# Performance work log

Hardware: AMD Instinct MI355X
Metric: run time of the kernel (lower is better)

The kernel has to match this reference:

```python
import jax, jax.numpy as jnp
import numpy as np

N, H, F, E, K = 4096, 512, 2048, 8, 2  # tokens, hidden, ffn(=4H), experts, top_k


def setup_inputs() -> dict:
    key = jax.random.key(0)
    ks = jax.random.split(key, 7)
    def w(k, shape, fan_in):
        return jax.random.normal(k, shape, dtype=jnp.float32) * (fan_in ** -0.5)
    return {
        "x": jax.random.normal(ks[0], (N, H), dtype=jnp.float32),
        "W_in": w(ks[1], (H, H), H),          # input_proj.weight  [out,in]
        "W_router": w(ks[2], (E, H), H),      # router.gate.weight [E,H]
        "W_gate": w(ks[3], (E, F, H), H),     # per-expert gate_proj.weight
        "W_up": w(ks[4], (E, F, H), H),       # per-expert up_proj.weight
        "W_down": w(ks[5], (E, H, F), F),     # per-expert down_proj.weight
        "W_out": w(ks[6], (H, H), H),         # output_proj.weight
    }


def reference(x, W_in, W_router, W_gate, W_up, W_down, W_out):
    h = x @ W_in.T                                  # [N,H] input_proj
    logits = h @ W_router.T                         # [N,E]
    # route_mode='balanced' and world_size==1 -> expert_bias is None
    probs = jax.nn.softmax(logits, axis=-1)
    top_w, top_i = jax.lax.top_k(probs, K)          # [N,K]
    top_w = jax.nn.softmax(top_w, axis=-1)          # renormalize over top-k

    # per-token combine weight for each expert: [N,E]
    onehot = jax.nn.one_hot(top_i, E, dtype=h.dtype)      # [N,K,E]
    combine_w = jnp.einsum('nk,nke->ne', top_w, onehot)

    def expert(wg, wu, wd):
        # SwiGLU FFN: down( silu(gate(h)) * up(h) )
        return (jax.nn.silu(h @ wg.T) * (h @ wu.T)) @ wd.T  # [N,H]

    expert_out = jax.vmap(expert)(W_gate, W_up, W_down)     # [E,N,H]
    combined = jnp.einsum('ne,enh->nh', combine_w, expert_out)
    return combined @ W_out.T                                # output_proj
```

## Files before the change

kernel.cpp:

```cpp
#include <hip/hip_runtime.h>

typedef unsigned short u16;
typedef unsigned int u32;
typedef short bf16x8 __attribute__((ext_vector_type(8)));
typedef float f32x4 __attribute__((ext_vector_type(4)));

#define AS1 __attribute__((address_space(1)))
#define AS3 __attribute__((address_space(3)))

#define NTOK 4096
#define HDIM 512
#define FDIM 2048
#define NEXP 8
#define NASSIGN (NTOK * 2)
#define NPAD (NASSIGN + NEXP * 128)
#define RBMAX 128

__device__ __forceinline__ void g2l16(const void* g, void* l) {
  __builtin_amdgcn_global_load_lds((const AS1 u32*)g, (AS3 u32*)l, 16, 0, 0);
}
__device__ __forceinline__ u16 f2bf(float f) {
  u32 u = __float_as_uint(f);
  u = (u + 0x7FFFu + ((u >> 16) & 1u)) >> 16;
  return (u16)u;
}
__device__ __forceinline__ float bf2f(u16 h) { return __uint_as_float(((u32)h) << 16); }

#define VMBAR() do { asm volatile("s_waitcnt vmcnt(0)" ::: "memory"); __builtin_amdgcn_s_barrier(); } while (0)

__global__ __launch_bounds__(512, 4) void prep1_kernel(
    const float* __restrict__ x, const float* __restrict__ Wi, const float* __restrict__ Wo,
    const float* __restrict__ Wr, u16* __restrict__ xb, u16* __restrict__ Wib,
    u16* __restrict__ Wob, double* __restrict__ wre) {
  const int b = blockIdx.x, tid = threadIdx.x;
  if (b < 640) {
    const float* s; u16* d; int base;
    if (b < 512) { s = x; d = xb; base = b * 1024; }
    else if (b < 576) { s = Wi; d = Wib; base = (b - 512) * 1024; }
    else { s = Wo; d = Wob; base = (b - 576) * 1024; }
#pragma unroll
    for (int i = 0; i < 2; ++i) {
      const int ix = base + tid + i * 512;
      const float4 v = ((const float4*)s)[ix];
      ushort4 o; o.x = f2bf(v.x); o.y = f2bf(v.y); o.z = f2bf(v.z); o.w = f2bf(v.w);
      ((ushort4*)d)[ix] = o;
    }
  } else {
    const int t = (b - 640) * 512 + tid;
    const int e = t >> 9, k = t & 511;
    const float* wr = Wr + e * HDIM;
    double a = 0.0;
    for (int j = 0; j < HDIM; ++j) a += (double)wr[j] * (double)Wi[j * HDIM + k];
    wre[t] = a;
  }
}

template <int SB, int NT>
__device__ __forceinline__ void gemm128_body(
    const u16* __restrict__ A, const u16* __restrict__ B, void* __restrict__ C,
    int m0, int n0, int N, int K, u16* sm, int tid) {
  u16 *lA0 = sm, *lA1 = sm + 8192, *lB0 = sm + 16384, *lB1 = sm + 24576;
  const int w = tid >> 6, l = tid & 63;
  const int wm = (w >> 2) * 64, wn = (w & 3) * 32;
  const int lm = l & 15, lk = (l >> 4) * 8, xr = (l & 7) << 3;
  const int sr = l >> 3, sc = ((l & 7) ^ sr) * 8;
  const u16* As = A + (size_t)(m0 + w * 8 + sr) * K + sc;
  const u16* Bs = B + (size_t)(n0 + w * 8 + sr) * K + sc;
  f32x4 acc[4][2] = {};
  auto STG = [&](u16* dA, u16* dB, int kt) {
    g2l16(As + kt, dA + w * 512);
    g2l16(As + (size_t)64 * K + kt, dA + 4096 + w * 512);
    g2l16(Bs + kt, dB + w * 512);
    g2l16(Bs + (size_t)64 * K + kt, dB + 4096 + w * 512);
  };
  auto CMP = [&](const u16* a_, const u16* b_) {
#pragma unroll
    for (int kk = 0; kk < 2; ++kk) {
      const int ko = (kk * 32 + lk) ^ xr;
      bf16x8 af[4], bf[2];
#pragma unroll
      for (int i = 0; i < 4; ++i) af[i] = *(const bf16x8*)(a_ + (wm + i * 16 + lm) * 64 + ko);
#pragma unroll
      for (int j = 0; j < 2; ++j) bf[j] = *(const bf16x8*)(b_ + (wn + j * 16 + lm) * 64 + ko);
#pragma unroll
      for (int i = 0; i < 4; ++i)
#pragma unroll
        for (int j = 0; j < 2; ++j)
          acc[i][j] = __builtin_amdgcn_mfma_f32_16x16x32_bf16(af[i], bf[j], acc[i][j], 0, 0, 0);
    }
  };
  STG(lA0, lB0, 0);
  VMBAR();
  for (int t = 0; t < NT; t += 2) {
    if (t + 1 < NT) STG(lA1, lB1, (t + 1) * 64);
    CMP(lA0, lB0);
    VMBAR();
    if (t + 2 < NT) STG(lA0, lB0, (t + 2) * 64);
    CMP(lA1, lB1);
    VMBAR();
  }
  const int cr = (l >> 4) * 4, cc = lm;
#pragma unroll
  for (int i = 0; i < 4; ++i)
#pragma unroll
    for (int j = 0; j < 2; ++j)
#pragma unroll
      for (int r = 0; r < 4; ++r) {
        const size_t o = (size_t)(m0 + wm + i * 16 + cr + r) * N + n0 + wn + j * 16 + cc;
        if (SB) ((u16*)C)[o] = f2bf(acc[i][j][r]);
        else ((float*)C)[o] = acc[i][j][r];
      }
}

__global__ __launch_bounds__(512, 4) void prep2_kernel(
    const float* __restrict__ x, const double* __restrict__ wre,
    const u16* __restrict__ xb, const u16* __restrict__ Wib,
    const float* __restrict__ Wg, const float* __restrict__ Wu, const float* __restrict__ Wd,
    u16* __restrict__ hb, u16* __restrict__ Wgb, u16* __restrict__ Wub, u16* __restrict__ Wdb,
    int* __restrict__ idx, float* __restrict__ wts) {
  __shared__ __align__(16) u16 pp[32768];
  const int b = blockIdx.x, tid = threadIdx.x;
  if (b < 8) {
    double* lw = (double*)pp;
    for (int i = tid; i < NEXP * HDIM; i += 512) lw[i] = wre[i];
    __syncthreads();
    const int n = b * 512 + tid;
    const float* xr = x + (size_t)n * HDIM;
    double acc[NEXP] = {};
    for (int k4 = 0; k4 < HDIM / 4; ++k4) {
      const float4 xv = ((const float4*)xr)[k4];
      const float xc[4] = {xv.x, xv.y, xv.z, xv.w};
#pragma unroll
      for (int c = 0; c < 4; ++c) {
        const double xd = (double)xc[c];
#pragma unroll
        for (int e = 0; e < NEXP; ++e) acc[e] += xd * lw[e * HDIM + k4 * 4 + c];
      }
    }
    double mx = acc[0];
#pragma unroll
    for (int e = 1; e < NEXP; ++e) mx = acc[e] > mx ? acc[e] : mx;
    double p[NEXP], se = 0.0;
#pragma unroll
    for (int e = 0; e < NEXP; ++e) { p[e] = exp(acc[e] - mx); se += p[e]; }
    const double inv = 1.0 / se;
#pragma unroll
    for (int e = 0; e < NEXP; ++e) p[e] *= inv;
    int i0 = 0; double b0 = p[0];
#pragma unroll
    for (int e = 1; e < NEXP; ++e) if (p[e] > b0) { b0 = p[e]; i0 = e; }
    int i1 = -1; double b1 = -1.0;
#pragma unroll
    for (int e = 0; e < NEXP; ++e) if (e != i0 && p[e] > b1) { b1 = p[e]; i1 = e; }
    const double e0 = exp(b0), e1 = exp(b1);
    idx[2 * n] = i0; idx[2 * n + 1] = i1;
    wts[2 * n] = (float)(e0 / (e0 + e1));
    wts[2 * n + 1] = (float)(e1 / (e0 + e1));
  } else if (b < 136) {
    const int g = b - 8;
    gemm128_body<1, 8>(xb, Wib, hb, (g >> 2) * 128, (g & 3) * 128, HDIM, HDIM, pp, tid);
  } else {
    const int cb = b - 136, which = cb >> 9, lb = cb & 511;
    const float* s = which == 0 ? Wg : which == 1 ? Wu : Wd;
    u16* d = which == 0 ? Wgb : which == 1 ? Wub : Wdb;
    const int base = lb * 4096 + tid;
#pragma unroll
    for (int i = 0; i < 8; ++i) {
      const int ix = base + i * 512;
      const float4 v = ((const float4*)s)[ix];
      ushort4 o; o.x = f2bf(v.x); o.y = f2bf(v.y); o.z = f2bf(v.z); o.w = f2bf(v.w);
      ((ushort4*)d)[ix] = o;
    }
  }
}

__global__ void assign_kernel(const int* __restrict__ idx, int* __restrict__ tok,
                              int* __restrict__ pos, int* __restrict__ rbe,
                              int* __restrict__ rbp, int* __restrict__ nrb) {
  __shared__ int cnt[NEXP], cur[NEXP];
  const int tid = threadIdx.x;
  if (tid < NEXP) cnt[tid] = 0;
  __syncthreads();
  for (int a = tid; a < NASSIGN; a += 256) atomicAdd(&cnt[idx[a]], 1);
  __syncthreads();
  if (tid == 0) {
    int o = 0, n = 0;
    for (int e = 0; e < NEXP; ++e) {
      cur[e] = o;
      const int nb = (cnt[e] + 127) >> 7;
      for (int i = 0; i < nb; ++i) { rbe[n] = e; rbp[n] = o + i * 128; ++n; }
      o += nb * 128;
    }
    nrb[0] = n;
  }
  __syncthreads();
  for (int p = tid; p < NPAD; p += 256) tok[p] = 0;
  __syncthreads();
  for (int a = tid; a < NASSIGN; a += 256) {
    const int e = idx[a];
    const int q = atomicAdd(&cur[e], 1);
    tok[q] = a >> 1;
    pos[a] = q;
  }
}

__global__ __launch_bounds__(512, 2) void gateup_kernel(
    const u16* __restrict__ hb, const u16* __restrict__ Wg, const u16* __restrict__ Wu,
    u16* __restrict__ act, const int* __restrict__ tok, const int* __restrict__ rbe,
    const int* __restrict__ rbp, const int* __restrict__ nrb) {
  const int rb = blockIdx.y;
  if (rb >= nrb[0]) return;
  __shared__ __align__(16) u16 sm[49152];
  u16 *lA0 = sm, *lA1 = sm + 8192, *lG0 = sm + 16384, *lG1 = sm + 24576,
      *lU0 = sm + 32768, *lU1 = sm + 40960;
  const int e = rbe[rb], p0 = rbp[rb], n0 = blockIdx.x * 128;
  const int tid = threadIdx.x, w = tid >> 6, l = tid & 63;
  const int wm = (w >> 2) * 64, wn = (w & 3) * 32;
  const int lm = l & 15, lk = (l >> 4) * 8, xr = (l & 7) << 3;
  const int sr = l >> 3, sc = ((l & 7) ^ sr) * 8;
  const u16* A0 = hb + (size_t)tok[p0 + w * 8 + sr] * HDIM + sc;
  const u16* A1 = hb + (size_t)tok[p0 + 64 + w * 8 + sr] * HDIM + sc;
  const u16* G0 = Wg + (size_t)e * FDIM * HDIM + (size_t)(n0 + w * 8 + sr) * HDIM + sc;
  const u16* G1 = G0 + (size_t)64 * HDIM;
  const u16* U0 = Wu + (size_t)e * FDIM * HDIM + (size_t)(n0 + w * 8 + sr) * HDIM + sc;
  const u16* U1 = U0 + (size_t)64 * HDIM;
  f32x4 ag[4][2] = {}, au[4][2] = {};
  auto STG = [&](u16* dA, u16* dG, u16* dU, int kt) {
    g2l16(A0 + kt, dA + w * 512);
    g2l16(A1 + kt, dA + 4096 + w * 512);
    g2l16(G0 + kt, dG + w * 512);
    g2l16(G1 + kt, dG + 4096 + w * 512);
    g2l16(U0 + kt, dU + w * 512);
    g2l16(U1 + kt, dU + 4096 + w * 512);
  };
  auto CMP = [&](const u16* a_, const u16* g_, const u16* u_) {
#pragma unroll
    for (int kk = 0; kk < 2; ++kk) {
      const int ko = (kk * 32 + lk) ^ xr;
      bf16x8 af[4], gf[2], uf[2];
#pragma unroll
      for (int i = 0; i < 4; ++i) af[i] = *(const bf16x8*)(a_ + (wm + i * 16 + lm) * 64 + ko);
#pragma unroll
      for (int j = 0; j < 2; ++j) {
        gf[j] = *(const bf16x8*)(g_ + (wn + j * 16 + lm) * 64 + ko);
        uf[j] = *(const bf16x8*)(u_ + (wn + j * 16 + lm) * 64 + ko);
      }
#pragma unroll
      for (int i = 0; i < 4; ++i)
#pragma unroll
        for (int j = 0; j < 2; ++j) {
          ag[i][j] = __builtin_amdgcn_mfma_f32_16x16x32_bf16(af[i], gf[j], ag[i][j], 0, 0, 0);
          au[i][j] = __builtin_amdgcn_mfma_f32_16x16x32_bf16(af[i], uf[j], au[i][j], 0, 0, 0);
        }
    }
  };
  STG(lA0, lG0, lU0, 0);
  VMBAR();
#pragma unroll
  for (int t = 0; t < 8; t += 2) {
    if (t + 1 < 8) STG(lA1, lG1, lU1, (t + 1) * 64);
    CMP(lA0, lG0, lU0);
    VMBAR();
    if (t + 2 < 8) STG(lA0, lG0, lU0, (t + 2) * 64);
    CMP(lA1, lG1, lU1);
    VMBAR();
  }
  const int cr = (l >> 4) * 4, cc = lm;
#pragma unroll
  for (int i = 0; i < 4; ++i)
#pragma unroll
    for (int j = 0; j < 2; ++j)
#pragma unroll
      for (int r = 0; r < 4; ++r) {
        const float g = ag[i][j][r], u = au[i][j][r];
        const float s = g / (1.0f + __expf(-g));
        act[(size_t)(p0 + wm + i * 16 + cr + r) * FDIM + n0 + wn + j * 16 + cc] = f2bf(s * u);
      }
}

__global__ __launch_bounds__(512, 2) void down_kernel(
    const u16* __restrict__ act, const u16* __restrict__ Wd, u16* __restrict__ dwn,
    const int* __restrict__ rbe, const int* __restrict__ rbp, const int* __restrict__ nrb) {
  const int rb = blockIdx.y;
  if (rb >= nrb[0]) return;
  __shared__ __align__(16) u16 sm[49152];
  u16 *lA0 = sm, *lA1 = sm + 8192, *lB0 = sm + 16384, *lB1 = sm + 32768;
  const int e = rbe[rb], p0 = rbp[rb], n0 = blockIdx.x * 256;
  const int tid = threadIdx.x, w = tid >> 6, l = tid & 63;
  const int wm = (w >> 2) * 64, wn = (w & 3) * 64;
  const int lm = l & 15, lk = (l >> 4) * 8, xr = (l & 7) << 3;
  const int sr = l >> 3, sc = ((l & 7) ^ sr) * 8;
  const u16* As = act + (size_t)(p0 + w * 8 + sr) * FDIM + sc;
  const u16* Bs = Wd + (size_t)e * HDIM * FDIM + (size_t)(n0 + w * 8 + sr) * FDIM + sc;
  f32x4 acc[4][4] = {};
  auto STG = [&](u16* dA, u16* dB, int kt) {
    g2l16(As + kt, dA + w * 512);
    g2l16(As + (size_t)64 * FDIM + kt, dA + 4096 + w * 512);
#pragma unroll
    for (int c = 0; c < 4; ++c)
      g2l16(Bs + (size_t)(64 * c) * FDIM + kt, dB + c * 4096 + w * 512);
  };
  auto CMP = [&](const u16* a_, const u16* b_) {
#pragma unroll
    for (int kk = 0; kk < 2; ++kk) {
      const int ko = (kk * 32 + lk) ^ xr;
      bf16x8 af[4], bf[4];
#pragma unroll
      for (int i = 0; i < 4; ++i) af[i] = *(const bf16x8*)(a_ + (wm + i * 16 + lm) * 64 + ko);
#pragma unroll
      for (int j = 0; j < 4; ++j) bf[j] = *(const bf16x8*)(b_ + (wn + j * 16 + lm) * 64 + ko);
#pragma unroll
      for (int i = 0; i < 4; ++i)
#pragma unroll
        for (int j = 0; j < 4; ++j)
          acc[i][j] = __builtin_amdgcn_mfma_f32_16x16x32_bf16(af[i], bf[j], acc[i][j], 0, 0, 0);
    }
  };
  STG(lA0, lB0, 0);
  VMBAR();
  for (int t = 0; t < 32; t += 2) {
    if (t + 1 < 32) STG(lA1, lB1, (t + 1) * 64);
    CMP(lA0, lB0);
    VMBAR();
    if (t + 2 < 32) STG(lA0, lB0, (t + 2) * 64);
    CMP(lA1, lB1);
    VMBAR();
  }
  const int cr = (l >> 4) * 4, cc = lm;
#pragma unroll
  for (int i = 0; i < 4; ++i)
#pragma unroll
    for (int j = 0; j < 4; ++j)
#pragma unroll
      for (int r = 0; r < 4; ++r)
        dwn[(size_t)(p0 + wm + i * 16 + cr + r) * HDIM + n0 + wn + j * 16 + cc] = f2bf(acc[i][j][r]);
}

__global__ void combine_kernel(const u16* __restrict__ dwn, const int* __restrict__ pos,
                               const float* __restrict__ wts, u16* __restrict__ cb) {
  const int n = blockIdx.x, t = threadIdx.x;
  const int p0 = pos[2 * n], p1 = pos[2 * n + 1];
  const float w0 = wts[2 * n], w1 = wts[2 * n + 1];
  const ushort4 a = ((const ushort4*)(dwn + (size_t)p0 * HDIM))[t];
  const ushort4 b = ((const ushort4*)(dwn + (size_t)p1 * HDIM))[t];
  ushort4 o;
  o.x = f2bf(w0 * bf2f(a.x) + w1 * bf2f(b.x));
  o.y = f2bf(w0 * bf2f(a.y) + w1 * bf2f(b.y));
  o.z = f2bf(w0 * bf2f(a.z) + w1 * bf2f(b.z));
  o.w = f2bf(w0 * bf2f(a.w) + w1 * bf2f(b.w));
  ((ushort4*)(cb + (size_t)n * HDIM))[t] = o;
}

__global__ __launch_bounds__(512, 4) void out_gemm_kernel(
    const u16* __restrict__ cb, const u16* __restrict__ Wob, float* __restrict__ out) {
  __shared__ __align__(16) u16 sm[32768];
  gemm128_body<0, 8>(cb, Wob, out, blockIdx.y * 128, blockIdx.x * 128, HDIM, HDIM, sm, threadIdx.x);
}

extern "C" void kernel_launch(void* const* d_in, const int* in_sizes, int n_in,
                              void* d_out, int out_size, void* d_ws, size_t ws_size,
                              hipStream_t stream) {
  const float* x  = (const float*)d_in[0];
  const float* Wi = (const float*)d_in[1];
  const float* Wr = (const float*)d_in[2];
  const float* Wg = (const float*)d_in[3];
  const float* Wu = (const float*)d_in[4];
  const float* Wd = (const float*)d_in[5];
  const float* Wo = (const float*)d_in[6];
  float* out = (float*)d_out;

  char* ws = (char*)d_ws;
  size_t off = 0;
  auto alloc = [&](size_t bytes) -> void* {
    off = (off + 255) & ~(size_t)255;
    void* p = ws + off;
    off += bytes;
    return p;
  };
  u16* xb  = (u16*)alloc((size_t)NTOK * HDIM * 2);
  u16* hb  = (u16*)alloc((size_t)NTOK * HDIM * 2);
  u16* cb  = (u16*)alloc((size_t)NTOK * HDIM * 2);
  u16* Wib = (u16*)alloc((size_t)HDIM * HDIM * 2);
  u16* Wob = (u16*)alloc((size_t)HDIM * HDIM * 2);
  u16* Wgb = (u16*)alloc((size_t)NEXP * FDIM * HDIM * 2);
  u16* Wub = (u16*)alloc((size_t)NEXP * FDIM * HDIM * 2);
  u16* Wdb = (u16*)alloc((size_t)NEXP * HDIM * FDIM * 2);
  u16* actb = (u16*)alloc((size_t)NPAD * FDIM * 2);
  u16* dwn = (u16*)alloc((size_t)NPAD * HDIM * 2);
  double* wre = (double*)alloc((size_t)NEXP * HDIM * 8);
  int* idx = (int*)alloc((size_t)NASSIGN * 4);
  float* wts = (float*)alloc((size_t)NASSIGN * 4);
  int* tok = (int*)alloc((size_t)NPAD * 4);
  int* pos = (int*)alloc((size_t)NASSIGN * 4);
  int* rbe = (int*)alloc((size_t)RBMAX * 4);
  int* rbp = (int*)alloc((size_t)RBMAX * 4);
  int* nrb = (int*)alloc(256);

  prep1_kernel<<<648, 512, 0, stream>>>(x, Wi, Wo, Wr, xb, Wib, Wob, wre);
  prep2_kernel<<<1672, 512, 0, stream>>>(x, wre, xb, Wib, Wg, Wu, Wd, hb, Wgb, Wub, Wdb, idx, wts);
  assign_kernel<<<1, 256, 0, stream>>>(idx, tok, pos, rbe, rbp, nrb);
  gateup_kernel<<<dim3(16, 72), 512, 0, stream>>>(hb, Wgb, Wub, actb, tok, rbe, rbp, nrb);
  down_kernel<<<dim3(2, 72), 512, 0, stream>>>(actb, Wdb, dwn, rbe, rbp, nrb);
  combine_kernel<<<NTOK, 128, 0, stream>>>(dwn, pos, wts, cb);
  out_gemm_kernel<<<dim3(4, 32), 512, 0, stream>>>(cb, Wob, out);
}
```

Measured before the change: 218.5 us.

## Restructure prep kernels, triple-buffer expert GEMMs, split-K down projection

Replaces the two mixed prep kernels with one flat conversion kernel, separate router-weight and router kernels, and a standalone input-projection GEMM. The gate/up and down GEMMs move from double to triple-buffered LDS staging with partial vmcnt waits, so loads stay in flight across an extra iteration. The down kernel is retiled to 128-wide output with an in-block split-K across two wave groups, reduced through LDS, doubling the grid. This adds more LDS per block and extra launches, and the reduction step adds overhead.

```diff
diff --git a/kernel.cpp b/kernel.cpp
--- a/kernel.cpp
+++ b/kernel.cpp
@@ -26,152 +26,86 @@
 }
 __device__ __forceinline__ float bf2f(u16 h) { return __uint_as_float(((u32)h) << 16); }
 
-#define VMBAR() do { asm volatile("s_waitcnt vmcnt(0)" ::: "memory"); __builtin_amdgcn_s_barrier(); } while (0)
-
-__global__ __launch_bounds__(512, 4) void prep1_kernel(
+#define WAITV6() asm volatile("s_waitcnt vmcnt(6)" ::: "memory")
+#define WAITV4() asm volatile("s_waitcnt vmcnt(4)" ::: "memory")
+#define WAITV0() asm volatile("s_waitcnt vmcnt(0)" ::: "memory")
+#define BAR() __builtin_amdgcn_s_barrier()
+#define VMBAR() do { WAITV0(); BAR(); } while (0)
+
+__global__ __launch_bounds__(256) void cvtall_kernel(
     const float* __restrict__ x, const float* __restrict__ Wi, const float* __restrict__ Wo,
-    const float* __restrict__ Wr, u16* __restrict__ xb, u16* __restrict__ Wib,
-    u16* __restrict__ Wob, double* __restrict__ wre) {
-  const int b = blockIdx.x, tid = threadIdx.x;
-  if (b < 640) {
-    const float* s; u16* d; int base;
-    if (b < 512) { s = x; d = xb; base = b * 1024; }
-    else if (b < 576) { s = Wi; d = Wib; base = (b - 512) * 1024; }
-    else { s = Wo; d = Wob; base = (b - 576) * 1024; }
-#pragma unroll
-    for (int i = 0; i < 2; ++i) {
-      const int ix = base + tid + i * 512;
-      const float4 v = ((const float4*)s)[ix];
-      ushort4 o; o.x = f2bf(v.x); o.y = f2bf(v.y); o.z = f2bf(v.z); o.w = f2bf(v.w);
-      ((ushort4*)d)[ix] = o;
+    const float* __restrict__ Wg, const float* __restrict__ Wu, const float* __restrict__ Wd,
+    u16* __restrict__ xb, u16* __restrict__ Wib, u16* __restrict__ Wob,
+    u16* __restrict__ Wgb, u16* __restrict__ Wub, u16* __restrict__ Wdb) {
+  const int gid = blockIdx.x * 256 + threadIdx.x;
+  const int S = 6784 * 256;
+#pragma unroll
+  for (int k = 0; k < 4; ++k) {
+    const int i = gid + k * S;
+    const float* s; u16* d; int o;
+    if (i < 524288) { s = x; d = xb; o = i; }
+    else if (i < 589824) { s = Wi; d = Wib; o = i - 524288; }
+    else if (i < 655360) { s = Wo; d = Wob; o = i - 589824; }
+    else if (i < 2752512) { s = Wg; d = Wgb; o = i - 655360; }
+    else if (i < 4849664) { s = Wu; d = Wub; o = i - 2752512; }
+    else { s = Wd; d = Wdb; o = i - 4849664; }
+    const float4 v = ((const float4*)s)[o];
+    ushort4 t; t.x = f2bf(v.x); t.y = f2bf(v.y); t.z = f2bf(v.z); t.w = f2bf(v.w);
+    ((ushort4*)d)[o] = t;
+  }
+}
+
+__global__ __launch_bounds__(256) void wreff_kernel(
+    const float* __restrict__ Wr, const float* __restrict__ Wi, double* __restrict__ wre) {
+  const int t = blockIdx.x * 256 + threadIdx.x;
+  const int e = t >> 9, k = t & 511;
+  const float* wr = Wr + e * HDIM;
+  double a = 0.0;
+  for (int j = 0; j < HDIM; j += 8) {
+#pragma unroll
+    for (int u = 0; u < 8; ++u) a += (double)wr[j + u] * (double)Wi[(j + u) * HDIM + k];
+  }
+  wre[t] = a;
+}
+
+__global__ __launch_bounds__(256) void router_kernel(
+    const float* __restrict__ x, const double* __restrict__ wre,
+    int* __restrict__ idx, float* __restrict__ wts) {
+  __shared__ double lw[NEXP * HDIM];
+  for (int i = threadIdx.x; i < NEXP * HDIM; i += 256) lw[i] = wre[i];
+  __syncthreads();
+  const int n = blockIdx.x * 256 + threadIdx.x;
+  const float* xr = x + (size_t)n * HDIM;
+  double acc[NEXP] = {};
+  for (int k4 = 0; k4 < HDIM / 4; ++k4) {
+    const float4 xv = ((const float4*)xr)[k4];
+    const float xc[4] = {xv.x, xv.y, xv.z, xv.w};
+#pragma unroll
+    for (int c = 0; c < 4; ++c) {
+      const double xd = (double)xc[c];
+#pragma unroll
+      for (int e = 0; e < NEXP; ++e) acc[e] += xd * lw[e * HDIM + k4 * 4 + c];
     }
-  } else {
-    const int t = (b - 640) * 512 + tid;
-    const int e = t >> 9, k = t & 511;
-    const float* wr = Wr + e * HDIM;
-    double a = 0.0;
-    for (int j = 0; j < HDIM; ++j) a += (double)wr[j] * (double)Wi[j * HDIM + k];
-    wre[t] = a;
-  }
-}
-
-template <int SB, int NT>
-__device__ __forceinline__ void gemm128_body(
-    const u16* __restrict__ A, const u16* __restrict__ B, void* __restrict__ C,
-    int m0, int n0, int N, int K, u16* sm, int tid) {
-  u16 *lA0 = sm, *lA1 = sm + 8192, *lB0 = sm + 16384, *lB1 = sm + 24576;
-  const int w = tid >> 6, l = tid & 63;
-  const int wm = (w >> 2) * 64, wn = (w & 3) * 32;
-  const int lm = l & 15, lk = (l >> 4) * 8, xr = (l & 7) << 3;
-  const int sr = l >> 3, sc = ((l & 7) ^ sr) * 8;
-  const u16* As = A + (size_t)(m0 + w * 8 + sr) * K + sc;
-  const u16* Bs = B + (size_t)(n0 + w * 8 + sr) * K + sc;
-  f32x4 acc[4][2] = {};
-  auto STG = [&](u16* dA, u16* dB, int kt) {
-    g2l16(As + kt, dA + w * 512);
-    g2l16(As + (size_t)64 * K + kt, dA + 4096 + w * 512);
-    g2l16(Bs + kt, dB + w * 512);
-    g2l16(Bs + (size_t)64 * K + kt, dB + 4096 + w * 512);
-  };
-  auto CMP = [&](const u16* a_, const u16* b_) {
-#pragma unroll
-    for (int kk = 0; kk < 2; ++kk) {
-      const int ko = (kk * 32 + lk) ^ xr;
-      bf16x8 af[4], bf[2];
-#pragma unroll
-      for (int i = 0; i < 4; ++i) af[i] = *(const bf16x8*)(a_ + (wm + i * 16 + lm) * 64 + ko);
-#pragma unroll
-      for (int j = 0; j < 2; ++j) bf[j] = *(const bf16x8*)(b_ + (wn + j * 16 + lm) * 64 + ko);
-#pragma unroll
-      for (int i = 0; i < 4; ++i)
-#pragma unroll
-        for (int j = 0; j < 2; ++j)
-          acc[i][j] = __builtin_amdgcn_mfma_f32_16x16x32_bf16(af[i], bf[j], acc[i][j], 0, 0, 0);
-    }
-  };
-  STG(lA0, lB0, 0);
-  VMBAR();
-  for (int t = 0; t < NT; t += 2) {
-    if (t + 1 < NT) STG(lA1, lB1, (t + 1) * 64);
-    CMP(lA0, lB0);
-    VMBAR();
-    if (t + 2 < NT) STG(lA0, lB0, (t + 2) * 64);
-    CMP(lA1, lB1);
-    VMBAR();
-  }
-  const int cr = (l >> 4) * 4, cc = lm;
-#pragma unroll
-  for (int i = 0; i < 4; ++i)
-#pragma unroll
-    for (int j = 0; j < 2; ++j)
-#pragma unroll
-      for (int r = 0; r < 4; ++r) {
-        const size_t o = (size_t)(m0 + wm + i * 16 + cr + r) * N + n0 + wn + j * 16 + cc;
-        if (SB) ((u16*)C)[o] = f2bf(acc[i][j][r]);
-        else ((float*)C)[o] = acc[i][j][r];
-      }
-}
-
-__global__ __launch_bounds__(512, 4) void prep2_kernel(
-    const float* __restrict__ x, const double* __restrict__ wre,
-    const u16* __restrict__ xb, const u16* __restrict__ Wib,
-    const float* __restrict__ Wg, const float* __restrict__ Wu, const float* __restrict__ Wd,
-    u16* __restrict__ hb, u16* __restrict__ Wgb, u16* __restrict__ Wub, u16* __restrict__ Wdb,
-    int* __restrict__ idx, float* __restrict__ wts) {
-  __shared__ __align__(16) u16 pp[32768];
-  const int b = blockIdx.x, tid = threadIdx.x;
-  if (b < 8) {
-    double* lw = (double*)pp;
-    for (int i = tid; i < NEXP * HDIM; i += 512) lw[i] = wre[i];
-    __syncthreads();
-    const int n = b * 512 + tid;
-    const float* xr = x + (size_t)n * HDIM;
-    double acc[NEXP] = {};
-    for (int k4 = 0; k4 < HDIM / 4; ++k4) {
-      const float4 xv = ((const float4*)xr)[k4];
-      const float xc[4] = {xv.x, xv.y, xv.z, xv.w};
-#pragma unroll
-      for (int c = 0; c < 4; ++c) {
-        const double xd = (double)xc[c];
-#pragma unroll
-        for (int e = 0; e < NEXP; ++e) acc[e] += xd * lw[e * HDIM + k4 * 4 + c];
-      }
-    }
-    double mx = acc[0];
-#pragma unroll
-    for (int e = 1; e < NEXP; ++e) mx = acc[e] > mx ? acc[e] : mx;
-    double p[NEXP], se = 0.0;
-#pragma unroll
-    for (int e = 0; e < NEXP; ++e) { p[e] = exp(acc[e] - mx); se += p[e]; }
-    const double inv = 1.0 / se;
-#pragma unroll
-    for (int e = 0; e < NEXP; ++e) p[e] *= inv;
-    int i0 = 0; double b0 = p[0];
-#pragma unroll
-    for (int e = 1; e < NEXP; ++e) if (p[e] > b0) { b0 = p[e]; i0 = e; }
-    int i1 = -1; double b1 = -1.0;
-#pragma unroll
-    for (int e = 0; e < NEXP; ++e) if (e != i0 && p[e] > b1) { b1 = p[e]; i1 = e; }
-    const double e0 = exp(b0), e1 = exp(b1);
-    idx[2 * n] = i0; idx[2 * n + 1] = i1;
-    wts[2 * n] = (float)(e0 / (e0 + e1));
-    wts[2 * n + 1] = (float)(e1 / (e0 + e1));
-  } else if (b < 136) {
-    const int g = b - 8;
-    gemm128_body<1, 8>(xb, Wib, hb, (g >> 2) * 128, (g & 3) * 128, HDIM, HDIM, pp, tid);
-  } else {
-    const int cb = b - 136, which = cb >> 9, lb = cb & 511;
-    const float* s = which == 0 ? Wg : which == 1 ? Wu : Wd;
-    u16* d = which == 0 ? Wgb : which == 1 ? Wub : Wdb;
-    const int base = lb * 4096 + tid;
-#pragma unroll
-    for (int i = 0; i < 8; ++i) {
-      const int ix = base + i * 512;
-      const float4 v = ((const float4*)s)[ix];
-      ushort4 o; o.x = f2bf(v.x); o.y = f2bf(v.y); o.z = f2bf(v.z); o.w = f2bf(v.w);
-      ((ushort4*)d)[ix] = o;
-    }
-  }
+  }
+  double mx = acc[0];
+#pragma unroll
+  for (int e = 1; e < NEXP; ++e) mx = acc[e] > mx ? acc[e] : mx;
+  double p[NEXP], se = 0.0;
+#pragma unroll
+  for (int e = 0; e < NEXP; ++e) { p[e] = exp(acc[e] - mx); se += p[e]; }
+  const double inv = 1.0 / se;
+#pragma unroll
+  for (int e = 0; e < NEXP; ++e) p[e] *= inv;
+  int i0 = 0; double b0 = p[0];
+#pragma unroll
+  for (int e = 1; e < NEXP; ++e) if (p[e] > b0) { b0 = p[e]; i0 = e; }
+  int i1 = -1; double b1 = -1.0;
+#pragma unroll
+  for (int e = 0; e < NEXP; ++e) if (e != i0 && p[e] > b1) { b1 = p[e]; i1 = e; }
+  const double e0 = exp(b0), e1 = exp(b1);
+  idx[2 * n] = i0; idx[2 * n + 1] = i1;
+  wts[2 * n] = (float)(e0 / (e0 + e1));
+  wts[2 * n + 1] = (float)(e1 / (e0 + e1));
 }
 
 __global__ void assign_kernel(const int* __restrict__ idx, int* __restrict__ tok,
@@ -204,15 +138,82 @@
   }
 }
 
+template <int SB, int NT>
+__device__ __forceinline__ void gemm128_body(
+    const u16* __restrict__ A, const u16* __restrict__ B, void* __restrict__ C,
+    int m0, int n0, int N, int K, u16* sm, int tid) {
+  u16 *lA0 = sm, *lA1 = sm + 8192, *lB0 = sm + 16384, *lB1 = sm + 24576;
+  const int w = tid >> 6, l = tid & 63;
+  const int wm = (w >> 2) * 64, wn = (w & 3) * 32;
+  const int lm = l & 15, lk = (l >> 4) * 8, xr = (l & 7) << 3;
+  const int sr = l >> 3, sc = ((l & 7) ^ sr) * 8;
+  const u16* As = A + (size_t)(m0 + w * 8 + sr) * K + sc;
+  const u16* Bs = B + (size_t)(n0 + w * 8 + sr) * K + sc;
+  f32x4 acc[4][2] = {};
+  auto STG = [&](u16* dA, u16* dB, int kt) {
+    g2l16(As + kt, dA + w * 512);
+    g2l16(As + (size_t)64 * K + kt, dA + 4096 + w * 512);
+    g2l16(Bs + kt, dB + w * 512);
+    g2l16(Bs + (size_t)64 * K + kt, dB + 4096 + w * 512);
+  };
+  auto CMP = [&](const u16* a_, const u16* b_) {
+#pragma unroll
+    for (int kk = 0; kk < 2; ++kk) {
+      const int ko = (kk * 32 + lk) ^ xr;
+      bf16x8 af[4], bf[2];
+#pragma unroll
+      for (int i = 0; i < 4; ++i) af[i] = *(const bf16x8*)(a_ + (wm + i * 16 + lm) * 64 + ko);
+#pragma unroll
+      for (int j = 0; j < 2; ++j) bf[j] = *(const bf16x8*)(b_ + (wn + j * 16 + lm) * 64 + ko);
+#pragma unroll
+      for (int i = 0; i < 4; ++i)
+#pragma unroll
+        for (int j = 0; j < 2; ++j)
+          acc[i][j] = __builtin_amdgcn_mfma_f32_16x16x32_bf16(af[i], bf[j], acc[i][j], 0, 0, 0);
+    }
+  };
+  STG(lA0, lB0, 0);
+  VMBAR();
+  for (int t = 0; t < NT; t += 2) {
+    if (t + 1 < NT) STG(lA1, lB1, (t + 1) * 64);
+    CMP(lA0, lB0);
+    VMBAR();
+    if (t + 2 < NT) STG(lA0, lB0, (t + 2) * 64);
+    CMP(lA1, lB1);
+    VMBAR();
+  }
+  const int cr = (l >> 4) * 4, cc = lm;
+#pragma unroll
+  for (int i = 0; i < 4; ++i)
+#pragma unroll
+    for (int j = 0; j < 2; ++j)
+#pragma unroll
+      for (int r = 0; r < 4; ++r) {
+        const size_t o = (size_t)(m0 + wm + i * 16 + cr + r) * N + n0 + wn + j * 16 + cc;
+        if (SB) ((u16*)C)[o] = f2bf(acc[i][j][r]);
+        else ((float*)C)[o] = acc[i][j][r];
+      }
+}
+
+__global__ __launch_bounds__(512, 2) void ingemm_kernel(
+    const u16* __restrict__ xb, const u16* __restrict__ Wib, u16* __restrict__ hb) {
+  __shared__ __align__(16) u16 sm[32768];
+  gemm128_body<1, 8>(xb, Wib, hb, blockIdx.y * 128, blockIdx.x * 128, HDIM, HDIM, sm, threadIdx.x);
+}
+
+__global__ __launch_bounds__(512, 2) void outgemm_kernel(
+    const u16* __restrict__ cb, const u16* __restrict__ Wob, float* __restrict__ out) {
+  __shared__ __align__(16) u16 sm[32768];
+  gemm128_body<0, 8>(cb, Wob, out, blockIdx.y * 128, blockIdx.x * 128, HDIM, HDIM, sm, threadIdx.x);
+}
+
 __global__ __launch_bounds__(512, 2) void gateup_kernel(
     const u16* __restrict__ hb, const u16* __restrict__ Wg, const u16* __restrict__ Wu,
     u16* __restrict__ act, const int* __restrict__ tok, const int* __restrict__ rbe,
     const int* __restrict__ rbp, const int* __restrict__ nrb) {
   const int rb = blockIdx.y;
   if (rb >= nrb[0]) return;
-  __shared__ __align__(16) u16 sm[49152];
-  u16 *lA0 = sm, *lA1 = sm + 8192, *lG0 = sm + 16384, *lG1 = sm + 24576,
-      *lU0 = sm + 32768, *lU1 = sm + 40960;
+  __shared__ __align__(16) u16 sm[73728];
   const int e = rbe[rb], p0 = rbp[rb], n0 = blockIdx.x * 128;
   const int tid = threadIdx.x, w = tid >> 6, l = tid & 63;
   const int wm = (w >> 2) * 64, wn = (w & 3) * 32;
@@ -225,15 +226,19 @@
   const u16* U0 = Wu + (size_t)e * FDIM * HDIM + (size_t)(n0 + w * 8 + sr) * HDIM + sc;
   const u16* U1 = U0 + (size_t)64 * HDIM;
   f32x4 ag[4][2] = {}, au[4][2] = {};
-  auto STG = [&](u16* dA, u16* dG, u16* dU, int kt) {
-    g2l16(A0 + kt, dA + w * 512);
-    g2l16(A1 + kt, dA + 4096 + w * 512);
-    g2l16(G0 + kt, dG + w * 512);
-    g2l16(G1 + kt, dG + 4096 + w * 512);
-    g2l16(U0 + kt, dU + w * 512);
-    g2l16(U1 + kt, dU + 4096 + w * 512);
-  };
-  auto CMP = [&](const u16* a_, const u16* g_, const u16* u_) {
+  auto STG = [&](int b, int kt) {
+    u16* d = sm + b * 24576;
+    g2l16(A0 + kt, d + w * 512);
+    g2l16(A1 + kt, d + 4096 + w * 512);
+    g2l16(G0 + kt, d + 8192 + w * 512);
+    g2l16(G1 + kt, d + 12288 + w * 512);
+    g2l16(U0 + kt, d + 16384 + w * 512);
+    g2l16(U1 + kt, d + 20480 + w * 512);
+  };
+  auto CMP = [&](int b) {
+    const u16* a_ = sm + b * 24576;
+    const u16* g_ = a_ + 8192;
+    const u16* u_ = a_ + 16384;
 #pragma unroll
     for (int kk = 0; kk < 2; ++kk) {
       const int ko = (kk * 32 + lk) ^ xr;
@@ -254,16 +259,14 @@
         }
     }
   };
-  STG(lA0, lG0, lU0, 0);
-  VMBAR();
-#pragma unroll
-  for (int t = 0; t < 8; t += 2) {
-    if (t + 1 < 8) STG(lA1, lG1, lU1, (t + 1) * 64);
-    CMP(lA0, lG0, lU0);
-    VMBAR();
-    if (t + 2 < 8) STG(lA0, lG0, lU0, (t + 2) * 64);
-    CMP(lA1, lG1, lU1);
-    VMBAR();
+  STG(0, 0); STG(1, 64);
+  WAITV6(); BAR();
+#pragma unroll
+  for (int t = 0; t < 8; ++t) {
+    if (t + 2 < 8) STG((t + 2) % 3, (t + 2) * 64);
+    CMP(t % 3);
+    if (t + 2 < 8) WAITV6(); else WAITV0();
+    BAR();
   }
   const int cr = (l >> 4) * 4, cc = lm;
 #pragma unroll
@@ -284,56 +287,71 @@
   const int rb = blockIdx.y;
   if (rb >= nrb[0]) return;
   __shared__ __align__(16) u16 sm[49152];
-  u16 *lA0 = sm, *lA1 = sm + 8192, *lB0 = sm + 16384, *lB1 = sm + 32768;
-  const int e = rbe[rb], p0 = rbp[rb], n0 = blockIdx.x * 256;
+  const int e = rbe[rb], p0 = rbp[rb], n0 = blockIdx.x * 128;
   const int tid = threadIdx.x, w = tid >> 6, l = tid & 63;
-  const int wm = (w >> 2) * 64, wn = (w & 3) * 64;
+  const int g = w >> 2;
+  const int wm = ((w >> 1) & 1) * 64, wn = (w & 1) * 64;
   const int lm = l & 15, lk = (l >> 4) * 8, xr = (l & 7) << 3;
+  const int ko = (g * 32 + lk) ^ xr;
   const int sr = l >> 3, sc = ((l & 7) ^ sr) * 8;
   const u16* As = act + (size_t)(p0 + w * 8 + sr) * FDIM + sc;
   const u16* Bs = Wd + (size_t)e * HDIM * FDIM + (size_t)(n0 + w * 8 + sr) * FDIM + sc;
   f32x4 acc[4][4] = {};
-  auto STG = [&](u16* dA, u16* dB, int kt) {
-    g2l16(As + kt, dA + w * 512);
-    g2l16(As + (size_t)64 * FDIM + kt, dA + 4096 + w * 512);
-#pragma unroll
-    for (int c = 0; c < 4; ++c)
-      g2l16(Bs + (size_t)(64 * c) * FDIM + kt, dB + c * 4096 + w * 512);
-  };
-  auto CMP = [&](const u16* a_, const u16* b_) {
-#pragma unroll
-    for (int kk = 0; kk < 2; ++kk) {
-      const int ko = (kk * 32 + lk) ^ xr;
-      bf16x8 af[4], bf[4];
-#pragma unroll
-      for (int i = 0; i < 4; ++i) af[i] = *(const bf16x8*)(a_ + (wm + i * 16 + lm) * 64 + ko);
-#pragma unroll
-      for (int j = 0; j < 4; ++j) bf[j] = *(const bf16x8*)(b_ + (wn + j * 16 + lm) * 64 + ko);
-#pragma unroll
-      for (int i = 0; i < 4; ++i)
-#pragma unroll
-        for (int j = 0; j < 4; ++j)
-          acc[i][j] = __builtin_amdgcn_mfma_f32_16x16x32_bf16(af[i], bf[j], acc[i][j], 0, 0, 0);
-    }
-  };
-  STG(lA0, lB0, 0);
-  VMBAR();
-  for (int t = 0; t < 32; t += 2) {
-    if (t + 1 < 32) STG(lA1, lB1, (t + 1) * 64);
-    CMP(lA0, lB0);
-    VMBAR();
-    if (t + 2 < 32) STG(lA0, lB0, (t + 2) * 64);
-    CMP(lA1, lB1);
-    VMBAR();
-  }
-  const int cr = (l >> 4) * 4, cc = lm;
-#pragma unroll
-  for (int i = 0; i < 4; ++i)
-#pragma unroll
-    for (int j = 0; j < 4; ++j)
-#pragma unroll
-      for (int r = 0; r < 4; ++r)
-        dwn[(size_t)(p0 + wm + i * 16 + cr + r) * HDIM + n0 + wn + j * 16 + cc] = f2bf(acc[i][j][r]);
+  auto STG = [&](int b, int kt) {
+    u16* d = sm + b * 16384;
+    g2l16(As + kt, d + w * 512);
+    g2l16(As + (size_t)64 * FDIM + kt, d + 4096 + w * 512);
+    g2l16(Bs + kt, d + 8192 + w * 512);
+    g2l16(Bs + (size_t)64 * FDIM + kt, d + 12288 + w * 512);
+  };
+  auto CMP = [&](int b) {
+    const u16* a_ = sm + b * 16384;
+    const u16* b_ = a_ + 8192;
+    bf16x8 af[4], bf[4];
+#pragma unroll
+    for (int i = 0; i < 4; ++i) af[i] = *(const bf16x8*)(a_ + (wm + i * 16 + lm) * 64 + ko);
+#pragma unroll
+    for (int j = 0; j < 4; ++j) bf[j] = *(const bf16x8*)(b_ + (wn + j * 16 + lm) * 64 + ko);
+#pragma unroll
+    for (int i = 0; i < 4; ++i)
+#pragma unroll
+      for (int j = 0; j < 4; ++j)
+        acc[i][j] = __builtin_amdgcn_mfma_f32_16x16x32_bf16(af[i], bf[j], acc[i][j], 0, 0, 0);
+  };
+  STG(0, 0); STG(1, 64);
+  WAITV4(); BAR();
+#pragma unroll
+  for (int t = 0; t < 32; ++t) {
+    if (t + 2 < 32) STG((t + 2) % 3, (t + 2) * 64);
+    CMP(t % 3);
+    if (t + 2 < 32) WAITV4(); else WAITV0();
+    BAR();
+  }
+  asm volatile("s_waitcnt lgkmcnt(0)" ::: "memory");
+  __builtin_amdgcn_sched_barrier(0);
+  BAR();
+  float* red = (float*)sm;
+  if (g == 1) {
+#pragma unroll
+    for (int i = 0; i < 4; ++i)
+#pragma unroll
+      for (int j = 0; j < 4; ++j)
+        *(f32x4*)&red[(w & 3) * 4096 + (i * 4 + j) * 256 + l * 4] = acc[i][j];
+  }
+  BAR();
+  if (g == 0) {
+    const int cr = (l >> 4) * 4, cc = lm;
+#pragma unroll
+    for (int i = 0; i < 4; ++i)
+#pragma unroll
+      for (int j = 0; j < 4; ++j) {
+        const f32x4 o = *(const f32x4*)&red[w * 4096 + (i * 4 + j) * 256 + l * 4];
+        const f32x4 s = acc[i][j] + o;
+#pragma unroll
+        for (int r = 0; r < 4; ++r)
+          dwn[(size_t)(p0 + wm + i * 16 + cr + r) * HDIM + n0 + wn + j * 16 + cc] = f2bf(s[r]);
+      }
+  }
 }
 
 __global__ void combine_kernel(const u16* __restrict__ dwn, const int* __restrict__ pos,
@@ -349,12 +367,6 @@
   o.z = f2bf(w0 * bf2f(a.z) + w1 * bf2f(b.z));
   o.w = f2bf(w0 * bf2f(a.w) + w1 * bf2f(b.w));
   ((ushort4*)(cb + (size_t)n * HDIM))[t] = o;
-}
-
-__global__ __launch_bounds__(512, 4) void out_gemm_kernel(
-    const u16* __restrict__ cb, const u16* __restrict__ Wob, float* __restrict__ out) {
-  __shared__ __align__(16) u16 sm[32768];
-  gemm128_body<0, 8>(cb, Wob, out, blockIdx.y * 128, blockIdx.x * 128, HDIM, HDIM, sm, threadIdx.x);
 }
 
 extern "C" void kernel_launch(void* const* d_in, const int* in_sizes, int n_in,
@@ -396,11 +408,13 @@
   int* rbp = (int*)alloc((size_t)RBMAX * 4);
   int* nrb = (int*)alloc(256);
 
-  prep1_kernel<<<648, 512, 0, stream>>>(x, Wi, Wo, Wr, xb, Wib, Wob, wre);
-  prep2_kernel<<<1672, 512, 0, stream>>>(x, wre, xb, Wib, Wg, Wu, Wd, hb, Wgb, Wub, Wdb, idx, wts);
+  cvtall_kernel<<<6784, 256, 0, stream>>>(x, Wi, Wo, Wg, Wu, Wd, xb, Wib, Wob, Wgb, Wub, Wdb);
+  wreff_kernel<<<16, 256, 0, stream>>>(Wr, Wi, wre);
+  router_kernel<<<16, 256, 0, stream>>>(x, wre, idx, wts);
   assign_kernel<<<1, 256, 0, stream>>>(idx, tok, pos, rbe, rbp, nrb);
+  ingemm_kernel<<<dim3(4, 32), 512, 0, stream>>>(xb, Wib, hb);
   gateup_kernel<<<dim3(16, 72), 512, 0, stream>>>(hb, Wgb, Wub, actb, tok, rbe, rbp, nrb);
-  down_kernel<<<dim3(2, 72), 512, 0, stream>>>(actb, Wdb, dwn, rbe, rbp, nrb);
+  down_kernel<<<dim3(4, 72), 512, 0, stream>>>(actb, Wdb, dwn, rbe, rbp, nrb);
   combine_kernel<<<NTOK, 128, 0, stream>>>(dwn, pos, wts, cb);
-  out_gemm_kernel<<<dim3(4, 32), 512, 0, stream>>>(cb, Wob, out);
-}
+  outgemm_kernel<<<dim3(4, 32), 512, 0, stream>>>(cb, Wob, out);
+}
```

Result: no change. 218.2 us (-0.1%).
